# Performance work log

Hardware: AMD Instinct MI355X
Metric: run time of the kernel (lower is better)

Reference implementation:

```python
import jax, jax.numpy as jnp
import numpy as np

EPS = 1e-05  # matches tf entropy epsilon


def setup_inputs() -> dict:
    key = jax.random.key(0)
    k1, k2 = jax.random.split(key)
    encodings = jax.random.normal(k1, (8192, 64), dtype=jnp.float32)
    categorical = jax.random.uniform(k2, (8192, 25), dtype=jnp.float32)
    return {"encodings": encodings, "categorical": categorical, "k": 15}


def reference(encodings, categorical, k):
    B = encodings.shape[0]
    n_components = categorical.shape[1]
    k = min(k, B // 4)  # layer clamps k to batch_size // 4

    hard_groups = jnp.argmax(categorical, axis=1)           # [B] int
    max_groups = jnp.max(categorical, axis=1)               # [B]

    # Batched brute-force kNN. tf.norm's sqrt is monotonic, so the strict
    # comparison `dist < kth_dist` is identical on squared distances; working
    # in squared space avoids sqrt(0) issues and an extra pass.
    sq = jnp.sum(encodings * encodings, axis=1)             # [B]
    d2 = sq[:, None] + sq[None, :] - 2.0 * (encodings @ encodings.T)
    d2 = jnp.maximum(d2, 0.0)                               # [B, B]

    # (k+1)-smallest distances per row (0-indexed k, self-distance included,
    # matching tf.gather(tf.sort(distances), k)).
    neg_topk, _ = jax.lax.top_k(-d2, k + 1)                 # [B, k+1]
    kth = -neg_topk[:, k]                                   # [B] k-th smallest

    mask = (d2 < kth[:, None]).astype(jnp.float32)          # [B, B] strict <

    # Per-row label histogram over the neighborhood: counts[i,c] = #neighbors
    # of i in cluster c. Zero bins contribute 0 to -sum(b*log(b+eps)), same as
    # tf.bincount's variable-length output.
    onehot = jax.nn.one_hot(hard_groups, n_components, dtype=jnp.float32)
    counts = mask @ onehot                                  # [B, n_components]
    n_i = jnp.sum(counts, axis=-1, keepdims=True)           # [B, 1]
    bins = counts / jnp.maximum(n_i, 1.0)
    neighbourhood_entropy = -jnp.sum(bins * jnp.log(bins + EPS), axis=-1)  # [B]

    # Global cluster-size entropy + number of populated clusters.
    gcounts = jnp.sum(onehot, axis=0)                       # [n_components]
    gbins = gcounts / jnp.float32(B)
    cluster_size_entropy = -jnp.sum(gbins * jnp.log(gbins + EPS))
    n_populated = jnp.sum(gcounts > 0).astype(jnp.float32)

    return encodings, neighbourhood_entropy, cluster_size_entropy, n_populated, max_groups
```

## Files before the change

### kernel.cpp

```cpp
#include <hip/hip_runtime.h>
#include <math.h>

#define Bsz    8192
#define Dd     64
#define NC     25
#define RT     16
#define WAVES  16
#define KCAP   16
#define EPSf   1e-5f
#define JMASK  2097151u

typedef short  short8  __attribute__((ext_vector_type(8)));
typedef float  floatx4 __attribute__((ext_vector_type(4)));


__device__ inline unsigned short f2bf(float x) {
    unsigned u = __float_as_uint(x);
    u += 0x7FFFu + ((u >> 16) & 1u);
    return (unsigned short)(u >> 16);
}
__device__ inline float bf2f(unsigned short h) { return __uint_as_float(((unsigned)h) << 16); }

__device__ inline void oesort16(unsigned* a) {
    #pragma unroll
    for (int p = 1; p < 16; p <<= 1) {
        #pragma unroll
        for (int k = p; k >= 1; k >>= 1) {
            #pragma unroll
            for (int j = (k & (p - 1)); j + k < 16; j += 2 * k) {
                #pragma unroll
                for (int i = 0; i < k; ++i) {
                    if (i + j + k < 16 &&
                        ((i + j) / (2 * p)) == ((i + j + k) / (2 * p))) {
                        unsigned x = a[i + j], y = a[i + j + k];
                        a[i + j]     = (x < y) ? x : y;
                        a[i + j + k] = (x < y) ? y : x;
                    }
                }
            }
        }
    }
}
__device__ inline void bclean16(unsigned* t) {
    #pragma unroll
    for (int j = 8; j > 0; j >>= 1)
        #pragma unroll
        for (int i = 0; i < 16; ++i) {
            int l = i ^ j;
            if (l > i) {
                unsigned x = t[i], y = t[l];
                t[i] = (x < y) ? x : y;
                t[l] = (x < y) ? y : x;
            }
        }
}
__device__ inline void bmerge16(unsigned* ls, const unsigned* b) {
    unsigned t[16];
    #pragma unroll
    for (int i = 0; i < 16; ++i) { unsigned x = ls[i], y = b[15 - i]; t[i] = (x < y) ? x : y; }
    bclean16(t);
    #pragma unroll
    for (int i = 0; i < 16; ++i) ls[i] = t[i];
}
__device__ inline void bmerge16_shfl(unsigned* ls, int mask) {
    unsigned t[16];
    #pragma unroll
    for (int i = 0; i < 16; ++i) {
        unsigned pv = (unsigned)__shfl_xor((int)ls[15 - i], mask);
        unsigned x = ls[i];
        t[i] = (x < pv) ? x : pv;
    }
    bclean16(t);
    #pragma unroll
    for (int i = 0; i < 16; ++i) ls[i] = t[i];
}

__device__ inline void compute_pair(
    short8 ah0, short8 ah1, short8 al0, short8 al1,
    short8 ch0, short8 ch1, short8 cl0, short8 cl1,
    uint4 sva, uint4 svb,
    const short8* bh, const short8* bl, float sqi,
    unsigned* cand, int off)
{
    floatx4 accA = (floatx4){0.f, 0.f, 0.f, 0.f};
    floatx4 accB = (floatx4){0.f, 0.f, 0.f, 0.f};
    accA = __builtin_amdgcn_mfma_f32_16x16x32_bf16(ah0, bh[0], accA, 0, 0, 0);
    accB = __builtin_amdgcn_mfma_f32_16x16x32_bf16(ch0, bh[0], accB, 0, 0, 0);
    accA = __builtin_amdgcn_mfma_f32_16x16x32_bf16(ah0, bl[0], accA, 0, 0, 0);
    accB = __builtin_amdgcn_mfma_f32_16x16x32_bf16(ch0, bl[0], accB, 0, 0, 0);
    accA = __builtin_amdgcn_mfma_f32_16x16x32_bf16(al0, bh[0], accA, 0, 0, 0);
    accB = __builtin_amdgcn_mfma_f32_16x16x32_bf16(cl0, bh[0], accB, 0, 0, 0);
    accA = __builtin_amdgcn_mfma_f32_16x16x32_bf16(ah1, bh[1], accA, 0, 0, 0);
    accB = __builtin_amdgcn_mfma_f32_16x16x32_bf16(ch1, bh[1], accB, 0, 0, 0);
    accA = __builtin_amdgcn_mfma_f32_16x16x32_bf16(ah1, bl[1], accA, 0, 0, 0);
    accB = __builtin_amdgcn_mfma_f32_16x16x32_bf16(ch1, bl[1], accB, 0, 0, 0);
    accA = __builtin_amdgcn_mfma_f32_16x16x32_bf16(al1, bh[1], accA, 0, 0, 0);
    accB = __builtin_amdgcn_mfma_f32_16x16x32_bf16(cl1, bh[1], accB, 0, 0, 0);

    unsigned sa[4] = {sva.x, sva.y, sva.z, sva.w};
    unsigned sb[4] = {svb.x, svb.y, svb.z, svb.w};
    #pragma unroll
    for (int r = 0; r < 4; ++r) {
        float d2a = fmaxf(sqi + __uint_as_float(sa[r] & ~31u) + accA[r], 0.f);
        cand[off + r]     = (__float_as_uint(d2a) & ~31u) | (sa[r] & 31u);
        float d2b = fmaxf(sqi + __uint_as_float(sb[r] & ~31u) + accB[r], 0.f);
        cand[off + 4 + r] = (__float_as_uint(d2b) & ~31u) | (sb[r] & 31u);
    }
}


__global__ __launch_bounds__(256) void pre_kernel(
    const float* __restrict__ enc, const float* __restrict__ cat,
    unsigned int* __restrict__ slab,
    char* __restrict__ enc1, char* __restrict__ enc2,
    float* __restrict__ out_max, float* __restrict__ out_enc)
{
    const int gid = blockIdx.x * 256 + threadIdx.x;
    const int p = gid >> 5, pr = gid & 31;

    float2 ev = ((const float2*)enc)[gid];
    ((float2*)out_enc)[gid] = ev;

    float s = ev.x * ev.x + ev.y * ev.y;
    #pragma unroll
    for (int m = 1; m < 32; m <<= 1) s += __shfl_xor(s, m, 32);

    {
        const int g = p >> 4, c15p = p & 15;
        const int d0 = 2 * pr, kh = d0 >> 5, q = (d0 >> 3) & 3, e0 = d0 & 7;
        const int base = g * 4096 + kh * 1024 + (q * 16 + c15p) * 16 + e0 * 2;
        unsigned short ha = f2bf(ev.x), hb = f2bf(ev.y);
        unsigned short la = f2bf(ev.x - bf2f(ha)), lb = f2bf(ev.y - bf2f(hb));
        *(unsigned*)(enc1 + base)        = (unsigned)ha | ((unsigned)hb << 16);
        *(unsigned*)(enc1 + base + 2048) = (unsigned)la | ((unsigned)lb << 16);
        float y0 = -2.f * ev.x, y1 = -2.f * ev.y;
        unsigned short hc = f2bf(y0), hd = f2bf(y1);
        unsigned short lc = f2bf(y0 - bf2f(hc)), ld = f2bf(y1 - bf2f(hd));
        *(unsigned*)(enc2 + base)        = (unsigned)hc | ((unsigned)hd << 16);
        *(unsigned*)(enc2 + base + 2048) = (unsigned)lc | ((unsigned)ld << 16);
    }
    float cv = (pr < NC) ? cat[p * NC + pr] : -1.f;
    int ci = pr;
    #pragma unroll
    for (int m = 1; m < 32; m <<= 1) {
        float ov = __shfl_xor(cv, m, 32);
        int   oi = __shfl_xor(ci, m, 32);
        if (ov > cv || (ov == cv && oi < ci)) { cv = ov; ci = oi; }
    }
    if (pr == 0) {
        out_max[p] = cv;
        slab[p] = (__float_as_uint(s) & ~31u) | (unsigned)ci;
    }
}

__global__ __launch_bounds__(1024, 8) void main_kernel(
    const char* __restrict__ enc1, const char* __restrict__ enc2,
    const unsigned int* __restrict__ slab, const int* __restrict__ kptr,
    float* __restrict__ out_ent, float* __restrict__ out_glob)
{
    __shared__ unsigned wl[WAVES * 16 * 17];
    __shared__ int cnt[32];

    const int tid  = threadIdx.x, bid = blockIdx.x;
    const int wv   = tid >> 6, lane = tid & 63;
    const int quad = (tid >> 4) & 3, c15 = tid & 15;
    const int rowbase = bid * RT;

    short8 bh[2], bl[2];
    {
        const char* ib = enc1 + (size_t)bid * 4096 + lane * 16;
        bh[0] = *(const short8*)(ib);
        bh[1] = *(const short8*)(ib + 1024);
        bl[0] = *(const short8*)(ib + 2048);
        bl[1] = *(const short8*)(ib + 3072);
    }
    const float sqi = __uint_as_float(slab[rowbase + c15] & ~31u);

    unsigned ls[KCAP];
    #pragma unroll
    for (int q = 0; q < KCAP; ++q) ls[q] = 0xFFFFFFFFu;
    unsigned cand[16];

    const char* jb = enc2 + lane * 16;
    unsigned jo = (unsigned)wv * 4096u;
    const unsigned* sp = slab + wv * 16 + quad * 4;

    short8 Ah0 = *(const short8*)(jb + jo);
    short8 Ah1 = *(const short8*)(jb + jo + 1024);
    short8 Al0 = *(const short8*)(jb + jo + 2048);
    short8 Al1 = *(const short8*)(jb + jo + 3072);
    short8 Ch0 = *(const short8*)(jb + jo + 65536);
    short8 Ch1 = *(const short8*)(jb + jo + 66560);
    short8 Cl0 = *(const short8*)(jb + jo + 67584);
    short8 Cl1 = *(const short8*)(jb + jo + 68608);
    uint4  Asva = *(const uint4*)(sp);
    uint4  Asvb = *(const uint4*)(sp + 256);

    for (int t = 0; t < 8; ++t) {
        jo = (jo + 131072u) & JMASK; sp += 512;
        short8 Bh0 = *(const short8*)(jb + jo);
        short8 Bh1 = *(const short8*)(jb + jo + 1024);
        short8 Bl0 = *(const short8*)(jb + jo + 2048);
        short8 Bl1 = *(const short8*)(jb + jo + 3072);
        short8 Dh0 = *(const short8*)(jb + jo + 65536);
        short8 Dh1 = *(const short8*)(jb + jo + 66560);
        short8 Dl0 = *(const short8*)(jb + jo + 67584);
        short8 Dl1 = *(const short8*)(jb + jo + 68608);
        uint4  Bsva = *(const uint4*)(sp);
        uint4  Bsvb = *(const uint4*)(sp + 256);
        compute_pair(Ah0, Ah1, Al0, Al1, Ch0, Ch1, Cl0, Cl1, Asva, Asvb,
                     bh, bl, sqi, cand, 0);
        jo = (jo + 131072u) & JMASK; sp += 512;
        Ah0 = *(const short8*)(jb + jo);
        Ah1 = *(const short8*)(jb + jo + 1024);
        Al0 = *(const short8*)(jb + jo + 2048);
        Al1 = *(const short8*)(jb + jo + 3072);
        Ch0 = *(const short8*)(jb + jo + 65536);
        Ch1 = *(const short8*)(jb + jo + 66560);
        Cl0 = *(const short8*)(jb + jo + 67584);
        Cl1 = *(const short8*)(jb + jo + 68608);
        Asva = *(const uint4*)(sp);
        Asvb = *(const uint4*)(sp + 256);
        compute_pair(Bh0, Bh1, Bl0, Bl1, Dh0, Dh1, Dl0, Dl1, Bsva, Bsvb,
                     bh, bl, sqi, cand, 8);
        oesort16(cand);
        bmerge16(ls, cand);
    }

    if (bid == 0) {
        if (tid < 32) cnt[tid] = 0;
        __syncthreads();
        for (int i = tid; i < Bsz; i += 1024) atomicAdd(&cnt[slab[i] & 31u], 1);
        __syncthreads();
        if (tid == 0) {
            float gent = 0.f, npop = 0.f;
            for (int i = 0; i < NC; ++i) {
                int g = cnt[i];
                if (g > 0) {
                    npop += 1.f;
                    float gb = (float)g / (float)Bsz;
                    gent -= gb * logf(gb + EPSf);
                }
            }
            out_glob[0] = gent;
            out_glob[1] = npop;
        }
        __syncthreads();
    }

    bmerge16_shfl(ls, 16);
    bmerge16_shfl(ls, 32);
    if (quad == 0) {
        #pragma unroll
        for (int q = 0; q < KCAP; ++q) wl[(wv * 16 + c15) * 17 + q] = ls[q];
    }
    __syncthreads();
    if (wv == 0) {
        const int row = tid >> 2, sub = tid & 3;
        unsigned A[16], Bv[16];
        #pragma unroll
        for (int i = 0; i < 16; ++i) A[i]  = wl[((4 * sub)     * 16 + row) * 17 + i];
        #pragma unroll
        for (int i = 0; i < 16; ++i) Bv[i] = wl[((4 * sub + 1) * 16 + row) * 17 + i];
        bmerge16(A, Bv);
        #pragma unroll
        for (int i = 0; i < 16; ++i) Bv[i] = wl[((4 * sub + 2) * 16 + row) * 17 + i];
        bmerge16(A, Bv);
        #pragma unroll
        for (int i = 0; i < 16; ++i) Bv[i] = wl[((4 * sub + 3) * 16 + row) * 17 + i];
        bmerge16(A, Bv);
        bmerge16_shfl(A, 1);
        bmerge16_shfl(A, 2);

        int kk = kptr[0];
        if (kk > Bsz / 4) kk = Bsz / 4;
        if (kk > KCAP - 1) kk = KCAP - 1;

        unsigned kth = A[15];
        #pragma unroll
        for (int q = 0; q < 16; ++q) if (q == kk) kth = A[q];
        int nn = 0;
        #pragma unroll
        for (int t = 0; t < 15; ++t) nn += (t < kk && A[t] < kth) ? 1 : 0;

        float inv = 1.f / (float)((nn > 0) ? nn : 1);
        float part = 0.f;
        #pragma unroll
        for (int a4 = 0; a4 < 4; ++a4) {
            int a = sub + 4 * a4;
            if (a < nn) {
                int la = (int)(A[a] & 31u);
                int c = 0;
                #pragma unroll
                for (int b = 0; b < 15; ++b) c += (b < nn && (int)(A[b] & 31u) == la) ? 1 : 0;
                part -= inv * logf((float)c * inv + EPSf);
            }
        }
        part += __shfl_xor(part, 1);
        part += __shfl_xor(part, 2);
        if (sub == 0) out_ent[rowbase + row] = part;
    }
}

extern "C" void kernel_launch(void* const* d_in, const int* in_sizes, int n_in,
                              void* d_out, int out_size, void* d_ws, size_t ws_size,
                              hipStream_t stream)
{
    const float* enc  = (const float*)d_in[0];
    const float* cat  = (const float*)d_in[1];
    const int*   kptr = (const int*)d_in[2];
    float* out = (float*)d_out;

    unsigned int* slab = (unsigned int*)d_ws;
    char*         enc1 = (char*)d_ws + 32768;
    char*         enc2 = (char*)d_ws + 2129920;

    float* out_enc  = out;
    float* out_ent  = out + Bsz * Dd;
    float* out_glob = out + Bsz * Dd + Bsz;
    float* out_max  = out + Bsz * Dd + Bsz + 2;

    pre_kernel<<<1024, 256, 0, stream>>>(enc, cat, slab, enc1, enc2, out_max, out_enc);
    main_kernel<<<Bsz / RT, 1024, 0, stream>>>(enc1, enc2, slab, kptr, out_ent, out_glob);
}
```

Baseline: 135.4 us.

## Split each row tile's column range across two 512-thread blocks with atomic handoff

Each 16-row tile is now processed by two blocks of 8 waves, each covering half of the columns. Partial top-16 lists go to a global pair buffer, and the second block to finish, detected through an atomic counter, merges them and computes the entropy. This doubles the grid and halves the block size, aiming for better CU load balance and a shorter in-block merge tail. The cost is global memory traffic, fences and atomics for the cross-block merge, plus flag resets in the pre kernel.

```diff
diff --git a/kernel.cpp b/kernel.cpp
--- a/kernel.cpp
+++ b/kernel.cpp
@@ -5,7 +5,7 @@
 #define Dd     64
 #define NC     25
 #define RT     16
-#define WAVES  16
+#define NIG    512
 #define KCAP   16
 #define EPSf   1e-5f
 #define JMASK  2097151u
@@ -111,12 +111,14 @@
 
 __global__ __launch_bounds__(256) void pre_kernel(
     const float* __restrict__ enc, const float* __restrict__ cat,
-    unsigned int* __restrict__ slab,
+    unsigned int* __restrict__ slab, unsigned int* __restrict__ flags,
     char* __restrict__ enc1, char* __restrict__ enc2,
     float* __restrict__ out_max, float* __restrict__ out_enc)
 {
     const int gid = blockIdx.x * 256 + threadIdx.x;
     const int p = gid >> 5, pr = gid & 31;
+
+    if (gid < NIG) flags[gid] = 0;
 
     float2 ev = ((const float2*)enc)[gid];
     ((float2*)out_enc)[gid] = ev;
@@ -153,22 +155,24 @@
     }
 }
 
-__global__ __launch_bounds__(1024, 8) void main_kernel(
+__global__ __launch_bounds__(512, 4) void main_kernel(
     const char* __restrict__ enc1, const char* __restrict__ enc2,
     const unsigned int* __restrict__ slab, const int* __restrict__ kptr,
+    unsigned int* __restrict__ pairbuf, unsigned int* __restrict__ flags,
     float* __restrict__ out_ent, float* __restrict__ out_glob)
 {
-    __shared__ unsigned wl[WAVES * 16 * 17];
+    __shared__ unsigned wl[8 * 16 * 17];
     __shared__ int cnt[32];
 
     const int tid  = threadIdx.x, bid = blockIdx.x;
+    const int ig   = bid >> 1, half = bid & 1;
     const int wv   = tid >> 6, lane = tid & 63;
     const int quad = (tid >> 4) & 3, c15 = tid & 15;
-    const int rowbase = bid * RT;
+    const int rowbase = ig * RT;
 
     short8 bh[2], bl[2];
     {
-        const char* ib = enc1 + (size_t)bid * 4096 + lane * 16;
+        const char* ib = enc1 + (size_t)ig * 4096 + lane * 16;
         bh[0] = *(const short8*)(ib);
         bh[1] = *(const short8*)(ib + 1024);
         bl[0] = *(const short8*)(ib + 2048);
@@ -182,45 +186,45 @@
     unsigned cand[16];
 
     const char* jb = enc2 + lane * 16;
-    unsigned jo = (unsigned)wv * 4096u;
-    const unsigned* sp = slab + wv * 16 + quad * 4;
+    unsigned jo = (unsigned)half * 1048576u + (unsigned)wv * 4096u;
+    const unsigned* sp = slab + half * 4096 + wv * 16 + quad * 4;
 
     short8 Ah0 = *(const short8*)(jb + jo);
     short8 Ah1 = *(const short8*)(jb + jo + 1024);
     short8 Al0 = *(const short8*)(jb + jo + 2048);
     short8 Al1 = *(const short8*)(jb + jo + 3072);
-    short8 Ch0 = *(const short8*)(jb + jo + 65536);
-    short8 Ch1 = *(const short8*)(jb + jo + 66560);
-    short8 Cl0 = *(const short8*)(jb + jo + 67584);
-    short8 Cl1 = *(const short8*)(jb + jo + 68608);
+    short8 Ch0 = *(const short8*)(jb + jo + 32768);
+    short8 Ch1 = *(const short8*)(jb + jo + 33792);
+    short8 Cl0 = *(const short8*)(jb + jo + 34816);
+    short8 Cl1 = *(const short8*)(jb + jo + 35840);
     uint4  Asva = *(const uint4*)(sp);
-    uint4  Asvb = *(const uint4*)(sp + 256);
+    uint4  Asvb = *(const uint4*)(sp + 128);
 
     for (int t = 0; t < 8; ++t) {
-        jo = (jo + 131072u) & JMASK; sp += 512;
+        jo = (jo + 65536u) & JMASK; sp += 256;
         short8 Bh0 = *(const short8*)(jb + jo);
         short8 Bh1 = *(const short8*)(jb + jo + 1024);
         short8 Bl0 = *(const short8*)(jb + jo + 2048);
         short8 Bl1 = *(const short8*)(jb + jo + 3072);
-        short8 Dh0 = *(const short8*)(jb + jo + 65536);
-        short8 Dh1 = *(const short8*)(jb + jo + 66560);
-        short8 Dl0 = *(const short8*)(jb + jo + 67584);
-        short8 Dl1 = *(const short8*)(jb + jo + 68608);
+        short8 Dh0 = *(const short8*)(jb + jo + 32768);
+        short8 Dh1 = *(const short8*)(jb + jo + 33792);
+        short8 Dl0 = *(const short8*)(jb + jo + 34816);
+        short8 Dl1 = *(const short8*)(jb + jo + 35840);
         uint4  Bsva = *(const uint4*)(sp);
-        uint4  Bsvb = *(const uint4*)(sp + 256);
+        uint4  Bsvb = *(const uint4*)(sp + 128);
         compute_pair(Ah0, Ah1, Al0, Al1, Ch0, Ch1, Cl0, Cl1, Asva, Asvb,
                      bh, bl, sqi, cand, 0);
-        jo = (jo + 131072u) & JMASK; sp += 512;
+        jo = (jo + 65536u) & JMASK; sp += 256;
         Ah0 = *(const short8*)(jb + jo);
         Ah1 = *(const short8*)(jb + jo + 1024);
         Al0 = *(const short8*)(jb + jo + 2048);
         Al1 = *(const short8*)(jb + jo + 3072);
-        Ch0 = *(const short8*)(jb + jo + 65536);
-        Ch1 = *(const short8*)(jb + jo + 66560);
-        Cl0 = *(const short8*)(jb + jo + 67584);
-        Cl1 = *(const short8*)(jb + jo + 68608);
+        Ch0 = *(const short8*)(jb + jo + 32768);
+        Ch1 = *(const short8*)(jb + jo + 33792);
+        Cl0 = *(const short8*)(jb + jo + 34816);
+        Cl1 = *(const short8*)(jb + jo + 35840);
         Asva = *(const uint4*)(sp);
-        Asvb = *(const uint4*)(sp + 256);
+        Asvb = *(const uint4*)(sp + 128);
         compute_pair(Bh0, Bh1, Bl0, Bl1, Dh0, Dh1, Dl0, Dl1, Bsva, Bsvb,
                      bh, bl, sqi, cand, 8);
         oesort16(cand);
@@ -230,7 +234,7 @@
     if (bid == 0) {
         if (tid < 32) cnt[tid] = 0;
         __syncthreads();
-        for (int i = tid; i < Bsz; i += 1024) atomicAdd(&cnt[slab[i] & 31u], 1);
+        for (int i = tid; i < Bsz; i += 512) atomicAdd(&cnt[slab[i] & 31u], 1);
         __syncthreads();
         if (tid == 0) {
             float gent = 0.f, npop = 0.f;
@@ -259,46 +263,55 @@
         const int row = tid >> 2, sub = tid & 3;
         unsigned A[16], Bv[16];
         #pragma unroll
-        for (int i = 0; i < 16; ++i) A[i]  = wl[((4 * sub)     * 16 + row) * 17 + i];
-        #pragma unroll
-        for (int i = 0; i < 16; ++i) Bv[i] = wl[((4 * sub + 1) * 16 + row) * 17 + i];
-        bmerge16(A, Bv);
-        #pragma unroll
-        for (int i = 0; i < 16; ++i) Bv[i] = wl[((4 * sub + 2) * 16 + row) * 17 + i];
-        bmerge16(A, Bv);
-        #pragma unroll
-        for (int i = 0; i < 16; ++i) Bv[i] = wl[((4 * sub + 3) * 16 + row) * 17 + i];
+        for (int i = 0; i < 16; ++i) A[i]  = wl[((2 * sub)     * 16 + row) * 17 + i];
+        #pragma unroll
+        for (int i = 0; i < 16; ++i) Bv[i] = wl[((2 * sub + 1) * 16 + row) * 17 + i];
         bmerge16(A, Bv);
         bmerge16_shfl(A, 1);
         bmerge16_shfl(A, 2);
 
-        int kk = kptr[0];
-        if (kk > Bsz / 4) kk = Bsz / 4;
-        if (kk > KCAP - 1) kk = KCAP - 1;
-
-        unsigned kth = A[15];
-        #pragma unroll
-        for (int q = 0; q < 16; ++q) if (q == kk) kth = A[q];
-        int nn = 0;
-        #pragma unroll
-        for (int t = 0; t < 15; ++t) nn += (t < kk && A[t] < kth) ? 1 : 0;
-
-        float inv = 1.f / (float)((nn > 0) ? nn : 1);
-        float part = 0.f;
-        #pragma unroll
-        for (int a4 = 0; a4 < 4; ++a4) {
-            int a = sub + 4 * a4;
-            if (a < nn) {
-                int la = (int)(A[a] & 31u);
-                int c = 0;
-                #pragma unroll
-                for (int b = 0; b < 15; ++b) c += (b < nn && (int)(A[b] & 31u) == la) ? 1 : 0;
-                part -= inv * logf((float)c * inv + EPSf);
+        unsigned* slot = pairbuf + (((unsigned)ig * 2u + (unsigned)half) * 16u + (unsigned)row) * 16u;
+        #pragma unroll
+        for (int i = 0; i < 16; ++i) if ((i >> 2) == sub) slot[i] = A[i];
+        __threadfence();
+        int old = 0;
+        if (tid == 0) old = (int)atomicAdd(&flags[ig], 1u);
+        old = __shfl(old, 0);
+        if (old == 1) {
+            __threadfence();
+            const unsigned* ps = pairbuf + (((unsigned)ig * 2u + (unsigned)(1 - half)) * 16u + (unsigned)row) * 16u;
+            #pragma unroll
+            for (int i = 0; i < 16; ++i) Bv[i] = ps[i];
+            bmerge16(A, Bv);
+
+            int kk = kptr[0];
+            if (kk > Bsz / 4) kk = Bsz / 4;
+            if (kk > KCAP - 1) kk = KCAP - 1;
+
+            unsigned kth = A[15];
+            #pragma unroll
+            for (int q = 0; q < 16; ++q) if (q == kk) kth = A[q];
+            int nn = 0;
+            #pragma unroll
+            for (int t = 0; t < 15; ++t) nn += (t < kk && A[t] < kth) ? 1 : 0;
+
+            float inv = 1.f / (float)((nn > 0) ? nn : 1);
+            float part = 0.f;
+            #pragma unroll
+            for (int a4 = 0; a4 < 4; ++a4) {
+                int a = sub + 4 * a4;
+                if (a < nn) {
+                    int la = (int)(A[a] & 31u);
+                    int c = 0;
+                    #pragma unroll
+                    for (int b = 0; b < 15; ++b) c += (b < nn && (int)(A[b] & 31u) == la) ? 1 : 0;
+                    part -= inv * logf((float)c * inv + EPSf);
+                }
             }
+            part += __shfl_xor(part, 1);
+            part += __shfl_xor(part, 2);
+            if (sub == 0) out_ent[rowbase + row] = part;
         }
-        part += __shfl_xor(part, 1);
-        part += __shfl_xor(part, 2);
-        if (sub == 0) out_ent[rowbase + row] = part;
     }
 }
 
@@ -311,15 +324,17 @@
     const int*   kptr = (const int*)d_in[2];
     float* out = (float*)d_out;
 
-    unsigned int* slab = (unsigned int*)d_ws;
-    char*         enc1 = (char*)d_ws + 32768;
-    char*         enc2 = (char*)d_ws + 2129920;
+    unsigned int* slab    = (unsigned int*)d_ws;
+    char*         enc1    = (char*)d_ws + 32768;
+    char*         enc2    = (char*)d_ws + 2129920;
+    unsigned int* flags   = (unsigned int*)((char*)d_ws + 4227072);
+    unsigned int* pairbuf = (unsigned int*)((char*)d_ws + 4229120);
 
     float* out_enc  = out;
     float* out_ent  = out + Bsz * Dd;
     float* out_glob = out + Bsz * Dd + Bsz;
     float* out_max  = out + Bsz * Dd + Bsz + 2;
 
-    pre_kernel<<<1024, 256, 0, stream>>>(enc, cat, slab, enc1, enc2, out_max, out_enc);
-    main_kernel<<<Bsz / RT, 1024, 0, stream>>>(enc1, enc2, slab, kptr, out_ent, out_glob);
-}
+    pre_kernel<<<1024, 256, 0, stream>>>(enc, cat, slab, flags, enc1, enc2, out_max, out_enc);
+    main_kernel<<<NIG * 2, 512, 0, stream>>>(enc1, enc2, slab, kptr, pairbuf, flags, out_ent, out_glob);
+}
```

Result: slower. 167.7 us (+23.9%).

## Replace manual double-buffered tile loop with simpler per-tile loads and 8-candidate merge

Applied to the files above, without the earlier changes.

Replaces the register double-buffered loop, which prefetched the next pair of 16-column tiles, with a non-unrolled loop that loads each tile just before its MFMAs. Each iteration now covers two tiles and produces 8 candidates. These are sorted with an 8-element network and merged into the top-16 list with a cheaper half merge that only compares the upper 8 slots. The intent is to cut register pressure and sorting work, at the cost of losing explicit load/compute overlap.

```diff
diff --git a/kernel.cpp b/kernel.cpp
--- a/kernel.cpp
+++ b/kernel.cpp
@@ -5,10 +5,8 @@
 #define Dd     64
 #define NC     25
 #define RT     16
-#define WAVES  16
 #define KCAP   16
 #define EPSf   1e-5f
-#define JMASK  2097151u
 
 typedef short  short8  __attribute__((ext_vector_type(8)));
 typedef float  floatx4 __attribute__((ext_vector_type(4)));
@@ -21,16 +19,16 @@
 }
 __device__ inline float bf2f(unsigned short h) { return __uint_as_float(((unsigned)h) << 16); }
 
-__device__ inline void oesort16(unsigned* a) {
-    #pragma unroll
-    for (int p = 1; p < 16; p <<= 1) {
+__device__ inline void oesort8(unsigned* a) {
+    #pragma unroll
+    for (int p = 1; p < 8; p <<= 1) {
         #pragma unroll
         for (int k = p; k >= 1; k >>= 1) {
             #pragma unroll
-            for (int j = (k & (p - 1)); j + k < 16; j += 2 * k) {
+            for (int j = (k & (p - 1)); j + k < 8; j += 2 * k) {
                 #pragma unroll
                 for (int i = 0; i < k; ++i) {
-                    if (i + j + k < 16 &&
+                    if (i + j + k < 8 &&
                         ((i + j) / (2 * p)) == ((i + j + k) / (2 * p))) {
                         unsigned x = a[i + j], y = a[i + j + k];
                         a[i + j]     = (x < y) ? x : y;
@@ -54,6 +52,16 @@
             }
         }
 }
+__device__ inline void bmerge16_8(unsigned* ls, const unsigned* c) {
+    unsigned t[16];
+    #pragma unroll
+    for (int i = 0; i < 8; ++i) t[i] = ls[i];
+    #pragma unroll
+    for (int m = 0; m < 8; ++m) { unsigned x = ls[8 + m], y = c[7 - m]; t[8 + m] = (x < y) ? x : y; }
+    bclean16(t);
+    #pragma unroll
+    for (int i = 0; i < 16; ++i) ls[i] = t[i];
+}
 __device__ inline void bmerge16(unsigned* ls, const unsigned* b) {
     unsigned t[16];
     #pragma unroll
@@ -75,36 +83,30 @@
     for (int i = 0; i < 16; ++i) ls[i] = t[i];
 }
 
-__device__ inline void compute_pair(
-    short8 ah0, short8 ah1, short8 al0, short8 al1,
-    short8 ch0, short8 ch1, short8 cl0, short8 cl1,
-    uint4 sva, uint4 svb,
-    const short8* bh, const short8* bl, float sqi,
-    unsigned* cand, int off)
-{
-    floatx4 accA = (floatx4){0.f, 0.f, 0.f, 0.f};
-    floatx4 accB = (floatx4){0.f, 0.f, 0.f, 0.f};
-    accA = __builtin_amdgcn_mfma_f32_16x16x32_bf16(ah0, bh[0], accA, 0, 0, 0);
-    accB = __builtin_amdgcn_mfma_f32_16x16x32_bf16(ch0, bh[0], accB, 0, 0, 0);
-    accA = __builtin_amdgcn_mfma_f32_16x16x32_bf16(ah0, bl[0], accA, 0, 0, 0);
-    accB = __builtin_amdgcn_mfma_f32_16x16x32_bf16(ch0, bl[0], accB, 0, 0, 0);
-    accA = __builtin_amdgcn_mfma_f32_16x16x32_bf16(al0, bh[0], accA, 0, 0, 0);
-    accB = __builtin_amdgcn_mfma_f32_16x16x32_bf16(cl0, bh[0], accB, 0, 0, 0);
-    accA = __builtin_amdgcn_mfma_f32_16x16x32_bf16(ah1, bh[1], accA, 0, 0, 0);
-    accB = __builtin_amdgcn_mfma_f32_16x16x32_bf16(ch1, bh[1], accB, 0, 0, 0);
-    accA = __builtin_amdgcn_mfma_f32_16x16x32_bf16(ah1, bl[1], accA, 0, 0, 0);
-    accB = __builtin_amdgcn_mfma_f32_16x16x32_bf16(ch1, bl[1], accB, 0, 0, 0);
-    accA = __builtin_amdgcn_mfma_f32_16x16x32_bf16(al1, bh[1], accA, 0, 0, 0);
-    accB = __builtin_amdgcn_mfma_f32_16x16x32_bf16(cl1, bh[1], accB, 0, 0, 0);
-
-    unsigned sa[4] = {sva.x, sva.y, sva.z, sva.w};
-    unsigned sb[4] = {svb.x, svb.y, svb.z, svb.w};
+__device__ __attribute__((always_inline)) inline void do_tile(
+    const char* __restrict__ enc2, const unsigned* __restrict__ slab,
+    int soff, int lane16, int quad4,
+    const short8* bh, const short8* bl, float sqi, unsigned* cand)
+{
+    const char* base = enc2 + soff;
+    short8 a0 = *(const short8*)(base + lane16);
+    short8 a2 = *(const short8*)(base + lane16 + 2048);
+    uint4  sv = *(const uint4*)(slab + (soff >> 8) + quad4);
+    floatx4 acc = (floatx4){0.f, 0.f, 0.f, 0.f};
+    acc = __builtin_amdgcn_mfma_f32_16x16x32_bf16(a0, bh[0], acc, 0, 0, 0);
+    acc = __builtin_amdgcn_mfma_f32_16x16x32_bf16(a0, bl[0], acc, 0, 0, 0);
+    acc = __builtin_amdgcn_mfma_f32_16x16x32_bf16(a2, bh[0], acc, 0, 0, 0);
+    short8 a1 = *(const short8*)(base + lane16 + 1024);
+    short8 a3 = *(const short8*)(base + lane16 + 3072);
+    acc = __builtin_amdgcn_mfma_f32_16x16x32_bf16(a1, bh[1], acc, 0, 0, 0);
+    acc = __builtin_amdgcn_mfma_f32_16x16x32_bf16(a1, bl[1], acc, 0, 0, 0);
+    acc = __builtin_amdgcn_mfma_f32_16x16x32_bf16(a3, bh[1], acc, 0, 0, 0);
+
+    unsigned s[4] = {sv.x, sv.y, sv.z, sv.w};
     #pragma unroll
     for (int r = 0; r < 4; ++r) {
-        float d2a = fmaxf(sqi + __uint_as_float(sa[r] & ~31u) + accA[r], 0.f);
-        cand[off + r]     = (__float_as_uint(d2a) & ~31u) | (sa[r] & 31u);
-        float d2b = fmaxf(sqi + __uint_as_float(sb[r] & ~31u) + accB[r], 0.f);
-        cand[off + 4 + r] = (__float_as_uint(d2b) & ~31u) | (sb[r] & 31u);
+        float d2 = fmaxf(sqi + __uint_as_float(s[r] & ~31u) + acc[r], 0.f);
+        cand[r] = (__float_as_uint(d2) & ~31u) | (s[r] & 31u);
     }
 }
 
@@ -158,17 +160,18 @@
     const unsigned int* __restrict__ slab, const int* __restrict__ kptr,
     float* __restrict__ out_ent, float* __restrict__ out_glob)
 {
-    __shared__ unsigned wl[WAVES * 16 * 17];
+    __shared__ unsigned wl[16 * 16 * 17];
     __shared__ int cnt[32];
 
     const int tid  = threadIdx.x, bid = blockIdx.x;
     const int wv   = tid >> 6, lane = tid & 63;
     const int quad = (tid >> 4) & 3, c15 = tid & 15;
     const int rowbase = bid * RT;
+    const int lane16 = lane * 16, quad4 = quad * 4;
 
     short8 bh[2], bl[2];
     {
-        const char* ib = enc1 + (size_t)bid * 4096 + lane * 16;
+        const char* ib = enc1 + (size_t)bid * 4096 + lane16;
         bh[0] = *(const short8*)(ib);
         bh[1] = *(const short8*)(ib + 1024);
         bl[0] = *(const short8*)(ib + 2048);
@@ -179,52 +182,17 @@
     unsigned ls[KCAP];
     #pragma unroll
     for (int q = 0; q < KCAP; ++q) ls[q] = 0xFFFFFFFFu;
-    unsigned cand[16];
-
-    const char* jb = enc2 + lane * 16;
-    unsigned jo = (unsigned)wv * 4096u;
-    const unsigned* sp = slab + wv * 16 + quad * 4;
-
-    short8 Ah0 = *(const short8*)(jb + jo);
-    short8 Ah1 = *(const short8*)(jb + jo + 1024);
-    short8 Al0 = *(const short8*)(jb + jo + 2048);
-    short8 Al1 = *(const short8*)(jb + jo + 3072);
-    short8 Ch0 = *(const short8*)(jb + jo + 65536);
-    short8 Ch1 = *(const short8*)(jb + jo + 66560);
-    short8 Cl0 = *(const short8*)(jb + jo + 67584);
-    short8 Cl1 = *(const short8*)(jb + jo + 68608);
-    uint4  Asva = *(const uint4*)(sp);
-    uint4  Asvb = *(const uint4*)(sp + 256);
-
-    for (int t = 0; t < 8; ++t) {
-        jo = (jo + 131072u) & JMASK; sp += 512;
-        short8 Bh0 = *(const short8*)(jb + jo);
-        short8 Bh1 = *(const short8*)(jb + jo + 1024);
-        short8 Bl0 = *(const short8*)(jb + jo + 2048);
-        short8 Bl1 = *(const short8*)(jb + jo + 3072);
-        short8 Dh0 = *(const short8*)(jb + jo + 65536);
-        short8 Dh1 = *(const short8*)(jb + jo + 66560);
-        short8 Dl0 = *(const short8*)(jb + jo + 67584);
-        short8 Dl1 = *(const short8*)(jb + jo + 68608);
-        uint4  Bsva = *(const uint4*)(sp);
-        uint4  Bsvb = *(const uint4*)(sp + 256);
-        compute_pair(Ah0, Ah1, Al0, Al1, Ch0, Ch1, Cl0, Cl1, Asva, Asvb,
-                     bh, bl, sqi, cand, 0);
-        jo = (jo + 131072u) & JMASK; sp += 512;
-        Ah0 = *(const short8*)(jb + jo);
-        Ah1 = *(const short8*)(jb + jo + 1024);
-        Al0 = *(const short8*)(jb + jo + 2048);
-        Al1 = *(const short8*)(jb + jo + 3072);
-        Ch0 = *(const short8*)(jb + jo + 65536);
-        Ch1 = *(const short8*)(jb + jo + 66560);
-        Cl0 = *(const short8*)(jb + jo + 67584);
-        Cl1 = *(const short8*)(jb + jo + 68608);
-        Asva = *(const uint4*)(sp);
-        Asvb = *(const uint4*)(sp + 256);
-        compute_pair(Bh0, Bh1, Bl0, Bl1, Dh0, Dh1, Dl0, Dl1, Bsva, Bsvb,
-                     bh, bl, sqi, cand, 8);
-        oesort16(cand);
-        bmerge16(ls, cand);
+
+    const int wvoff = __builtin_amdgcn_readfirstlane(wv * 4096);
+
+    #pragma unroll 1
+    for (int m = 0; m < 16; ++m) {
+        unsigned cand[8];
+        const int soff = wvoff + m * 131072;
+        do_tile(enc2, slab, soff,          lane16, quad4, bh, bl, sqi, cand);
+        do_tile(enc2, slab, soff + 65536,  lane16, quad4, bh, bl, sqi, cand + 4);
+        oesort8(cand);
+        bmerge16_8(ls, cand);
     }
 
     if (bid == 0) {
```

After: 124.7 us. 7.9% less time.
